# Performance work log

Measured on AMD Instinct MI355X. Metric: run time of the kernel, lower is better.

## Reference

```python
import jax, jax.numpy as jnp
import numpy as np

B, L, D, H = 2, 2048, 2048, 16
HD = D // H          # head_dim = 128
LD = HD // 4         # latent_dim = 32


def _linear_params(key, fan_in, fan_out):
    kw, kb = jax.random.split(key)
    bound = 1.0 / np.sqrt(fan_in)
    W = jax.random.uniform(kw, (fan_in, fan_out), jnp.float32, -bound, bound)
    b = jax.random.uniform(kb, (fan_out,), jnp.float32, -bound, bound)
    return W, b


def setup_inputs() -> dict:
    key = jax.random.key(0)
    ks = jax.random.split(key, 12)
    x = jax.random.normal(ks[0], (B, L, D), jnp.float32)
    cos = jax.random.uniform(ks[1], (L, HD // 2), jnp.float32)
    sin = jax.random.uniform(ks[2], (L, HD // 2), jnp.float32)
    Wq, bq = _linear_params(ks[3], D, D)
    Wk, bk = _linear_params(ks[4], D, D)
    Wv, bv = _linear_params(ks[5], D, D)
    Wqc, bqc = _linear_params(ks[6], HD, LD)
    Wkc, bkc = _linear_params(ks[7], HD, LD)
    Wvc, bvc = _linear_params(ks[8], HD, LD)
    Wd, bd = _linear_params(ks[9], LD, HD)
    Wo, bo = _linear_params(ks[10], D, D)
    return dict(x=x, cos=cos, sin=sin, Wq=Wq, bq=bq, Wk=Wk, bk=bk, Wv=Wv, bv=bv,
                Wqc=Wqc, bqc=bqc, Wkc=Wkc, bkc=bkc, Wvc=Wvc, bvc=bvc,
                Wd=Wd, bd=bd, Wo=Wo, bo=bo)


def _apply_rope(q, k, cos, sin):
    # q, k: (B, H, L, HD); cos, sin: (L, HD//2) -> broadcast over B, H
    c = cos[None, None, :, :]
    s = sin[None, None, :, :]
    qe, qo = q[..., ::2], q[..., 1::2]
    ke, ko = k[..., ::2], k[..., 1::2]
    q_rot = jnp.stack([qe * c - qo * s, qe * s + qo * c], axis=-1).reshape(q.shape)
    k_rot = jnp.stack([ke * c - ko * s, ke * s + ko * c], axis=-1).reshape(k.shape)
    return q_rot, k_rot


def reference(x, cos, sin, Wq, bq, Wk, bk, Wv, bv,
              Wqc, bqc, Wkc, bkc, Wvc, bvc, Wd, bd, Wo, bo):
    b, l, d = x.shape
    # projections -> (B, H, L, HD)
    q = (x @ Wq + bq).reshape(b, l, H, HD).transpose(0, 2, 1, 3)
    k = (x @ Wk + bk).reshape(b, l, H, HD).transpose(0, 2, 1, 3)
    v = (x @ Wv + bv).reshape(b, l, H, HD).transpose(0, 2, 1, 3)
    q, k = _apply_rope(q, k, cos, sin)
    # low-rank compression into latent_dim
    qc = jnp.einsum('bhld,de->bhle', q, Wqc) + bqc
    kc = jnp.einsum('bhld,de->bhle', k, Wkc) + bkc
    vc = jnp.einsum('bhld,de->bhle', v, Wvc) + bvc
    scores = jnp.einsum('bhqe,bhke->bhqk', qc, kc) / np.sqrt(LD).astype(np.float32)
    causal = jnp.tril(jnp.ones((l, l), dtype=bool))  # True = keep
    scores = jnp.where(causal[None, None], scores, -jnp.inf)
    probs = jax.nn.softmax(scores, axis=-1)
    attn = jnp.einsum('bhqk,bhke->bhqe', probs, vc)
    attn = jnp.einsum('bhle,ed->bhld', attn, Wd) + bd  # decompress to HD
    attn = attn.transpose(0, 2, 1, 3).reshape(b, l, d)
    return attn @ Wo + bo
```

## Files before the change

### kernel.cpp

```cpp
#include <hip/hip_runtime.h>
#include <hip/hip_bf16.h>


#define Bsz 2
#define Lseq 2048
#define Dmod 2048
#define Hn 16
#define HDim 128
#define LDim 32

typedef __bf16 bf16x8 __attribute__((ext_vector_type(8)));
typedef float f32x4 __attribute__((ext_vector_type(4)));
typedef __hip_bfloat16 bf16;

#define GLDS16(g, l)                                                    \
  __builtin_amdgcn_global_load_lds(                                     \
      (const __attribute__((address_space(1))) unsigned int*)(g),       \
      (__attribute__((address_space(3))) unsigned int*)(l), 16, 0, 0)

#define SM_COS 0
#define SM_SIN 131072
#define SM_WC 262144
#define SM_BC 274432
#define SM_WD 274528
#define SM_BD 278624
#define SM_BO 278752
#define SM_BQKV 280800
#define SM_TOT 286944

__device__ inline void conv8(const void* src, size_t so, bf16* dst, size_t dof, int f32) {
  if (f32) {
    const float* s = (const float*)src + so;
    bf16 tmp[8] __attribute__((aligned(16)));
    for (int j = 0; j < 8; ++j) tmp[j] = __float2bfloat16(s[j]);
    *(uint4*)&dst[dof] = *(uint4*)tmp;
  } else {
    *(uint4*)&dst[dof] = *(const uint4*)((const ushort*)src + so);
  }
}

__device__ inline float cv1(const void* s, size_t i, int f32) {
  return f32 ? ((const float*)s)[i] : __bfloat162float(((const bf16*)s)[i]);
}

#define PB_FBP 0
#define PB_T3 256
#define PB_WV 3328
#define PB_CX 5376
#define PB_SM 9472
#define NB_PREP_ALL 9632

__global__ __launch_bounds__(256) void prep_all(
    const void* xS, const void* cosS, const void* sinS, const void* WqS,
    const void* WkS, const void* WvS, const void* WoS, const void* WqcS,
    const void* WkcS, const void* WvcS, const void* bqcS, const void* bkcS,
    const void* bvcS, const void* WdS, const void* bdS, const void* boS,
    const void* bqS, const void* bkS, const void* bvS,
    bf16* __restrict__ xb, bf16* __restrict__ WvB, bf16* __restrict__ WtQK,
    bf16* __restrict__ WtO, bf16* __restrict__ small, bf16* __restrict__ wctG,
    float* __restrict__ bo_part, int* __restrict__ flagW) {
  __shared__ __align__(16) char shm[16640];
  __shared__ int sflag;
  int blk = blockIdx.x;
  int t = threadIdx.x;

  if (t < 64) {
    int bad = 0;
    for (int k = 0; k < 4; ++k) {
      ushort u = ((const ushort*)xS)[t * 4 + k];
      int ex = (u >> 7) & 0xFF;
      if (ex >= 0xC0) bad = 1;
    }
    unsigned long long bl = __ballot(bad);
    if (t == 0) sflag = (bl != 0ULL) ? 1 : 0;
  }
  __syncthreads();
  int f32 = sflag;
  if (blk == 0 && t == 0) *flagW = f32;

  if (blk < PB_T3) {
    float* red = (float*)shm;
    int nb = blk & 15, kb = blk >> 4;
    int col = nb * 128 + (t & 127);
    int half = t >> 7;
    float s = 0.f;
    int kbase = kb * 128 + half * 64;
    for (int i = 0; i < 64; ++i) {
      int k = kbase + i;
      s += cv1(bdS, k & 127, f32) * cv1(WoS, (size_t)k * 2048 + col, f32);
    }
    red[t] = s;
    __syncthreads();
    if (half == 0) bo_part[kb * 2048 + col] = red[t] + red[t + 128];
  } else if (blk < PB_WV) {
    float (*tile)[65] = (float(*)[65])shm;
    int rem0 = blk - PB_T3;
    int z = rem0 >> 10, rem = rem0 & 1023;
    const void* W = (z == 0) ? WqS : (z == 1) ? WkS : WoS;
    bf16* Wt = (z == 2) ? WtO : (WtQK + (size_t)z * 2048 * 2048);
    int n0 = (rem & 31) * 64, k0 = (rem >> 5) * 64;
    int x = (t & 7) * 8, y = t >> 3;
    for (int p = 0; p < 2; ++p) {
      int r = y + p * 32;
      if (f32) {
        const float* src = (const float*)W + (size_t)(k0 + r) * 2048 + n0 + x;
        float4 a = *(const float4*)src;
        float4 b2 = *(const float4*)(src + 4);
        tile[r][x + 0] = a.x; tile[r][x + 1] = a.y; tile[r][x + 2] = a.z; tile[r][x + 3] = a.w;
        tile[r][x + 4] = b2.x; tile[r][x + 5] = b2.y; tile[r][x + 6] = b2.z; tile[r][x + 7] = b2.w;
      } else {
        const ushort* src = (const ushort*)W + (size_t)(k0 + r) * 2048 + n0 + x;
        uint4 u = *(const uint4*)src;
        bf16* e = (bf16*)&u;
        for (int jj = 0; jj < 8; ++jj) tile[r][x + jj] = __bfloat162float(e[jj]);
      }
    }
    __syncthreads();
    for (int p = 0; p < 2; ++p) {
      int n = y + p * 32;
      bf16 tmp[8] __attribute__((aligned(16)));
      for (int jj = 0; jj < 8; ++jj) tmp[jj] = __float2bfloat16(tile[x + jj][n]);
      *(uint4*)&Wt[(size_t)(n0 + n) * 2048 + k0 + x] = *(uint4*)tmp;
    }
  } else if (blk < PB_CX) {
    size_t e = ((size_t)(blk - PB_WV) * 256 + t) * 8;
    conv8(WvS, e, WvB, e, f32);
  } else if (blk < PB_SM) {
    size_t e = ((size_t)(blk - PB_CX) * 256 + t) * 8;
    conv8(xS, e, xb, e, f32);
  } else {
    int tid = (blk - PB_SM) * 256 + t;
    if (tid < SM_TOT / 8) {
      size_t e = (size_t)tid * 8;
      const void* src;
      size_t so;
      if (e < SM_SIN) { src = cosS; so = e - SM_COS; }
      else if (e < SM_WC) { src = sinS; so = e - SM_SIN; }
      else if (e < SM_BC) { size_t r = e - SM_WC; src = (r < 4096) ? WqcS : (r < 8192) ? WkcS : WvcS; so = r & 4095; }
      else if (e < SM_WD) { size_t r = e - SM_BC; src = (r < 32) ? bqcS : (r < 64) ? bkcS : bvcS; so = r & 31; }
      else if (e < SM_BD) { src = WdS; so = e - SM_WD; }
      else if (e < SM_BO) { src = bdS; so = e - SM_BD; }
      else if (e < SM_BQKV) { src = boS; so = e - SM_BO; }
      else { size_t r = e - SM_BQKV; src = (r < 2048) ? bqS : (r < 4096) ? bkS : bvS; so = r & 2047; }
      conv8(src, so, small, e, f32);
    } else {
      int idx = tid - SM_TOT / 8;
      for (int i = idx; i < 12288; i += 40960 - SM_TOT / 8) {
        int reg = i >> 12, rem2 = i & 4095, n = rem2 >> 7, k = rem2 & 127;
        const void* src = (reg == 0) ? WqcS : (reg == 1) ? WkcS : WvcS;
        wctG[i] = __float2bfloat16(cv1(src, (size_t)k * 32 + n, f32));
      }
    }
  }
}

__global__ __launch_bounds__(256) void fold_all(
    const bf16* __restrict__ WvB, const bf16* __restrict__ wctG,
    const bf16* __restrict__ WtO, const bf16* __restrict__ small,
    const void* boS, const float* __restrict__ bo_part, const void* bvS,
    const void* bvcS, const void* WvcS, bf16* __restrict__ Wvt,
    bf16* __restrict__ Wot, float* __restrict__ boF, float* __restrict__ bvF,
    const int* __restrict__ flagp) {
  int blk = blockIdx.x;
  int t = threadIdx.x, lane = t & 63, w = t >> 6;
  int qd = lane >> 4, ln = lane & 15;
  if (blk < 256) {
    int nb = blk & 15, h = blk >> 4;
    f32x4 acc[2][2] = {};
    for (int kt = 0; kt < 4; ++kt) {
      bf16x8 af[2], bfr[2];
      for (int i = 0; i < 2; ++i)
        af[i] = *(const bf16x8*)&wctG[8192 + (i * 16 + ln) * 128 + kt * 32 + qd * 8];
      for (int j = 0; j < 2; ++j)
        bfr[j] = *(const bf16x8*)&WvB[(size_t)(nb * 128 + w * 32 + j * 16 + ln) * 2048 +
                                      h * 128 + kt * 32 + qd * 8];
      for (int i = 0; i < 2; ++i)
        for (int j = 0; j < 2; ++j)
          acc[i][j] = __builtin_amdgcn_mfma_f32_16x16x32_bf16(af[i], bfr[j], acc[i][j], 0, 0, 0);
    }
    for (int i = 0; i < 2; ++i)
      for (int j = 0; j < 2; ++j)
        for (int r = 0; r < 4; ++r) {
          int e = i * 16 + qd * 4 + r;
          int col = nb * 128 + w * 32 + j * 16 + ln;
          Wvt[(size_t)(h * 32 + e) * 2048 + col] = __float2bfloat16(acc[i][j][r]);
        }
  } else if (blk < 512) {
    int rem = blk - 256;
    int mb = rem & 15, h = rem >> 4;
    f32x4 acc[2][2] = {};
    for (int kt = 0; kt < 4; ++kt) {
      bf16x8 af[2], bfr[2];
      for (int i = 0; i < 2; ++i)
        af[i] = *(const bf16x8*)&WtO[(size_t)(mb * 128 + w * 32 + i * 16 + ln) * 2048 +
                                     h * 128 + kt * 32 + qd * 8];
      for (int j = 0; j < 2; ++j)
        bfr[j] = *(const bf16x8*)&small[SM_WD + (j * 16 + ln) * 128 + kt * 32 + qd * 8];
      for (int i = 0; i < 2; ++i)
        for (int j = 0; j < 2; ++j)
          acc[i][j] = __builtin_amdgcn_mfma_f32_16x16x32_bf16(af[i], bfr[j], acc[i][j], 0, 0, 0);
    }
    for (int i = 0; i < 2; ++i)
      for (int j = 0; j < 2; ++j)
        for (int r = 0; r < 4; ++r) {
          int row = mb * 128 + w * 32 + i * 16 + qd * 4 + r;
          int col = h * 32 + j * 16 + ln;
          Wot[(size_t)row * 512 + col] = __float2bfloat16(acc[i][j][r]);
        }
  } else {
    int f32 = *flagp;
    int tid = (blk - 512) * 256 + t;
    if (tid < 2048) {
      float s = cv1(boS, tid, f32);
      for (int kb = 0; kb < 16; ++kb) s += bo_part[kb * 2048 + tid];
      boF[tid] = s;
    } else if (tid < 2560) {
      int j = tid - 2048, h = j >> 5, e = j & 31;
      float s = cv1(bvcS, e, f32);
      for (int hd = 0; hd < 128; ++hd)
        s += cv1(bvS, h * 128 + hd, f32) * cv1(WvcS, (size_t)hd * 32 + e, f32);
      bvF[j] = s;
    }
  }
}

#define ESTR 136
__global__ __launch_bounds__(256) void gemm_qkv(
    const bf16* __restrict__ A, const bf16* __restrict__ Bt,
    const bf16* __restrict__ Wvt, const bf16* __restrict__ small,
    const bf16* __restrict__ wctG, const float* __restrict__ bvF,
    bf16* __restrict__ qc, bf16* __restrict__ kc, bf16* __restrict__ vcT) {
  __shared__ bf16 sh[128 * ESTR];
  const int K = 2048;
  int id = blockIdx.x;
  int t = threadIdx.x;
  int lane = t & 63, w = t >> 6;
  int qd = lane >> 4, ln = lane & 15;
  bf16* lA = sh;
  bf16* lB = sh + 4096;
  int wm = (w >> 1) * 64, wn = (w & 1) * 64;

  if (id < 1024) {
    int bn = id & 31, bm = id >> 5;
    int reg = bn >> 4, h = bn & 15;

    f32x4 acc[4][4] = {};
    const bf16* Ab = A + (size_t)(bm * 128) * K;
    const bf16* Bb = Bt + (size_t)(bn * 128) * K;

    for (int kt = 0; kt < K; kt += 32) {
      for (int p = 0; p < 2; ++p) {
        int slot = t + p * 256;
        int r = slot >> 2, c = (slot & 3) * 8;
        GLDS16(&Ab[(size_t)r * K + kt + c], &lA[slot * 8]);
        GLDS16(&Bb[(size_t)r * K + kt + c], &lB[slot * 8]);
      }
      __syncthreads();
      bf16x8 af[4], bfr[4];
      for (int i = 0; i < 4; ++i) af[i] = *(bf16x8*)&lA[(wm + i * 16 + ln) * 32 + qd * 8];
      for (int j = 0; j < 4; ++j) bfr[j] = *(bf16x8*)&lB[(wn + j * 16 + ln) * 32 + qd * 8];
      for (int i = 0; i < 4; ++i)
        for (int j = 0; j < 4; ++j)
          acc[i][j] = __builtin_amdgcn_mfma_f32_16x16x32_bf16(af[i], bfr[j], acc[i][j], 0, 0, 0);
      __syncthreads();
    }

    for (int j = 0; j < 4; ++j) {
      int col = wn + j * 16 + ln;
      float bv = __bfloat162float(small[SM_BQKV + bn * 128 + col]);
      for (int i = 0; i < 4; ++i)
        for (int r = 0; r < 4; ++r)
          sh[(wm + i * 16 + qd * 4 + r) * ESTR + col] = __float2bfloat16(acc[i][j][r] + bv);
    }
    __syncthreads();

    int r0 = w * 32;
    int b = bm >> 4;
    int bh = b * Hn + h;
    bf16x8 bfr2[2][4];
    for (int nt = 0; nt < 2; ++nt)
      for (int kt = 0; kt < 4; ++kt)
        bfr2[nt][kt] = *(const bf16x8*)&wctG[reg * 4096 + (nt * 16 + ln) * 128 + kt * 32 + qd * 8];
    float bc[2];
    bc[0] = __bfloat162float(small[SM_BC + reg * 32 + ln]);
    bc[1] = __bfloat162float(small[SM_BC + reg * 32 + 16 + ln]);

    for (int mt = 0; mt < 2; ++mt) {
      int lb = r0 + mt * 16 + ln;
      int lg2 = (bm & 15) * 128 + lb;
      f32x4 c2[2] = {};
      for (int kt = 0; kt < 4; ++kt) {
        uint4 u = *(uint4*)&sh[lb * ESTR + kt * 32 + qd * 8];
        bf16* e8 = (bf16*)&u;
        int pbase = kt * 16 + qd * 4;
        uint2 cu = *(const uint2*)&small[SM_COS + (size_t)lg2 * 64 + pbase];
        uint2 su = *(const uint2*)&small[SM_SIN + (size_t)lg2 * 64 + pbase];
        const bf16* cp = (const bf16*)&cu;
        const bf16* sp = (const bf16*)&su;
        for (int j = 0; j < 4; ++j) {
          float cvv = __bfloat162float(cp[j]);
          float svv = __bfloat162float(sp[j]);
          float ev = __bfloat162float(e8[2 * j]);
          float ov = __bfloat162float(e8[2 * j + 1]);
          e8[2 * j] = __float2bfloat16(ev * cvv - ov * svv);
          e8[2 * j + 1] = __float2bfloat16(ev * svv + ov * cvv);
        }
        bf16x8 a = *(bf16x8*)&u;
        c2[0] = __builtin_amdgcn_mfma_f32_16x16x32_bf16(a, bfr2[0][kt], c2[0], 0, 0, 0);
        c2[1] = __builtin_amdgcn_mfma_f32_16x16x32_bf16(a, bfr2[1][kt], c2[1], 0, 0, 0);
      }
      int lgbase = (bm & 15) * 128 + r0 + mt * 16 + qd * 4;
      bf16* dst = (reg == 0) ? qc : kc;
      for (int nt = 0; nt < 2; ++nt)
        for (int r = 0; r < 4; ++r)
          dst[((size_t)bh * Lseq + lgbase + r) * 32 + nt * 16 + ln] =
              __float2bfloat16(c2[nt][r] + bc[nt]);
    }
  } else {
    int rem = id - 1024;
    int nb = rem & 3, bm = rem >> 2;

    f32x4 acc[4][4] = {};
    const bf16* Ab = A + (size_t)(bm * 128) * K;
    const bf16* Bb = Wvt + (size_t)(nb * 128) * K;

    for (int kt = 0; kt < K; kt += 32) {
      for (int p = 0; p < 2; ++p) {
        int slot = t + p * 256;
        int r = slot >> 2, c = (slot & 3) * 8;
        GLDS16(&Ab[(size_t)r * K + kt + c], &lA[slot * 8]);
        GLDS16(&Bb[(size_t)r * K + kt + c], &lB[slot * 8]);
      }
      __syncthreads();
      bf16x8 af[4], bfr[4];
      for (int i = 0; i < 4; ++i) af[i] = *(bf16x8*)&lA[(wm + i * 16 + ln) * 32 + qd * 8];
      for (int j = 0; j < 4; ++j) bfr[j] = *(bf16x8*)&lB[(wn + j * 16 + ln) * 32 + qd * 8];
      for (int i = 0; i < 4; ++i)
        for (int j = 0; j < 4; ++j)
          acc[i][j] = __builtin_amdgcn_mfma_f32_16x16x32_bf16(af[i], bfr[j], acc[i][j], 0, 0, 0);
      __syncthreads();
    }

    int b = bm >> 4;
    for (int j = 0; j < 4; ++j) {
      int n = nb * 128 + wn + j * 16 + ln;
      float bb = bvF[n];
      for (int i = 0; i < 4; ++i) {
        int lloc = (bm & 15) * 128 + wm + i * 16 + qd * 4;
        bf16 p4[4] __attribute__((aligned(8)));
        for (int rr = 0; rr < 4; ++rr) p4[rr] = __float2bfloat16(acc[i][j][rr] + bb);
        *(uint2*)&vcT[((size_t)(b * 512 + n)) * 2048 + lloc] = *(uint2*)p4;
      }
    }
  }
}

__global__ __launch_bounds__(256) void gemm_bias_out(const bf16* __restrict__ A,
                                                     const bf16* __restrict__ Bt,
                                                     const float* __restrict__ bias,
                                                     void* __restrict__ C,
                                                     int M, int N, int K,
                                                     const int* __restrict__ flagp) {
  __shared__ bf16 lA[128 * 32];
  __shared__ bf16 lB[128 * 32];
  int f32out = *flagp;
  int bm = blockIdx.y, bn = blockIdx.x;
  int t = threadIdx.x;
  int lane = t & 63, w = t >> 6;
  int wm = (w >> 1) * 64, wn = (w & 1) * 64;
  int qd = lane >> 4, ln = lane & 15;

  f32x4 acc[4][4] = {};
  const bf16* Ab = A + (size_t)(bm * 128) * K;
  const bf16* Bb = Bt + (size_t)(bn * 128) * K;

  for (int kt = 0; kt < K; kt += 32) {
    for (int p = 0; p < 2; ++p) {
      int slot = t + p * 256;
      int r = slot >> 2, c = (slot & 3) * 8;
      GLDS16(&Ab[(size_t)r * K + kt + c], &lA[slot * 8]);
      GLDS16(&Bb[(size_t)r * K + kt + c], &lB[slot * 8]);
    }
    __syncthreads();
    bf16x8 af[4], bfr[4];
    for (int i = 0; i < 4; ++i) af[i] = *(bf16x8*)&lA[(wm + i * 16 + ln) * 32 + qd * 8];
    for (int j = 0; j < 4; ++j) bfr[j] = *(bf16x8*)&lB[(wn + j * 16 + ln) * 32 + qd * 8];
    for (int i = 0; i < 4; ++i)
      for (int j = 0; j < 4; ++j)
        acc[i][j] = __builtin_amdgcn_mfma_f32_16x16x32_bf16(af[i], bfr[j], acc[i][j], 0, 0, 0);
    __syncthreads();
  }
  for (int i = 0; i < 4; ++i)
    for (int j = 0; j < 4; ++j) {
      int col = bn * 128 + wn + j * 16 + ln;
      float bv = bias[col];
      for (int r = 0; r < 4; ++r) {
        int row = bm * 128 + wm + i * 16 + qd * 4 + r;
        float v = acc[i][j][r] + bv;
        if (f32out) ((float*)C)[(size_t)row * N + col] = v;
        else ((bf16*)C)[(size_t)row * N + col] = __float2bfloat16(v);
      }
    }
}

__global__ __launch_bounds__(256) void flash32(const bf16* __restrict__ qc,
                                               const bf16* __restrict__ kc,
                                               const bf16* __restrict__ vcT,
                                               bf16* __restrict__ attn) {
  __shared__ bf16 pbuf[4][16 * 72];
  __shared__ float oL[4][16][33];
  __shared__ float mL[4][16];
  __shared__ float lsL[4][16];
  int t = threadIdx.x;
  int lane = t & 63, w = t >> 6;
  int qd = lane >> 4, ln = lane & 15;
  int blk = blockIdx.x;
  int j = blk & 127;
  int bh = blk >> 7, h = bh & 15, b = bh >> 4;
  int q0 = j * 16;

  bf16x8 qf = *(const bf16x8*)&qc[((size_t)bh * Lseq + q0 + ln) * 32 + qd * 8];

  f32x4 o0 = {}, o1 = {};
  float m[4], ls[4];
  for (int r = 0; r < 4; ++r) { m[r] = -1e30f; ls[r] = 0.f; }
  const float scale2 = 0.17677669529663687f * 1.4426950408889634f;

  int n64 = (q0 + 16 + 63) >> 6;
  int nw = (n64 + 3) >> 2;
  int c0 = w * nw;
  int c1 = min(c0 + nw, n64);

  bf16* pb = pbuf[w];
  bf16x8 kf[4];
  if (c0 < c1) {
    int k0 = c0 * 64;
    for (int c = 0; c < 4; ++c)
      kf[c] = *(const bf16x8*)&kc[((size_t)bh * Lseq + k0 + c * 16 + ln) * 32 + qd * 8];
  }
  for (int ci = c0; ci < c1; ++ci) {
    int k0 = ci * 64;
    f32x4 s[4];
    __builtin_amdgcn_s_setprio(1);
    for (int c = 0; c < 4; ++c) {
      f32x4 z = {};
      s[c] = __builtin_amdgcn_mfma_f32_16x16x32_bf16(qf, kf[c], z, 0, 0, 0);
    }
    __builtin_amdgcn_s_setprio(0);
    size_t vbase = ((size_t)bh * 32 + ln) * Lseq + k0 + qd * 8;
    bf16x8 vf00 = *(const bf16x8*)&vcT[vbase];
    bf16x8 vf01 = *(const bf16x8*)&vcT[vbase + 32];
    bf16x8 vf10 = *(const bf16x8*)&vcT[vbase + (size_t)16 * Lseq];
    bf16x8 vf11 = *(const bf16x8*)&vcT[vbase + (size_t)16 * Lseq + 32];
    if (ci + 1 < c1) {
      int k0n = k0 + 64;
      for (int c = 0; c < 4; ++c)
        kf[c] = *(const bf16x8*)&kc[((size_t)bh * Lseq + k0n + c * 16 + ln) * 32 + qd * 8];
    }
    float sv[4][4];
    for (int r = 0; r < 4; ++r) {
      int qrow = q0 + qd * 4 + r;
      for (int c = 0; c < 4; ++c)
        sv[c][r] = (k0 + c * 16 + ln <= qrow) ? s[c][r] * scale2 : -1e30f;
    }
    for (int r = 0; r < 4; ++r) {
      float mx = fmaxf(fmaxf(sv[0][r], sv[1][r]), fmaxf(sv[2][r], sv[3][r]));
      for (int off = 1; off < 16; off <<= 1) mx = fmaxf(mx, __shfl_xor(mx, off, 64));
      if (!__all(mx <= m[r] + 8.f)) {
        float mn = fmaxf(m[r], mx);
        float alpha = exp2f(m[r] - mn);
        m[r] = mn;
        ls[r] *= alpha;
        o0[r] *= alpha;
        o1[r] *= alpha;
      }
      float rs = 0.f;
      for (int c = 0; c < 4; ++c) { sv[c][r] = exp2f(sv[c][r] - m[r]); rs += sv[c][r]; }
      ls[r] += rs;
    }
    for (int r = 0; r < 4; ++r)
      for (int c = 0; c < 4; ++c)
        pb[(qd * 4 + r) * 72 + c * 16 + ln] = __float2bfloat16(sv[c][r]);
    asm volatile("s_waitcnt lgkmcnt(0)" ::: "memory");
    bf16x8 pf0 = *(bf16x8*)&pb[ln * 72 + qd * 8];
    bf16x8 pf1 = *(bf16x8*)&pb[ln * 72 + 32 + qd * 8];
    __builtin_amdgcn_s_setprio(1);
    o0 = __builtin_amdgcn_mfma_f32_16x16x32_bf16(pf0, vf00, o0, 0, 0, 0);
    o0 = __builtin_amdgcn_mfma_f32_16x16x32_bf16(pf1, vf01, o0, 0, 0, 0);
    o1 = __builtin_amdgcn_mfma_f32_16x16x32_bf16(pf0, vf10, o1, 0, 0, 0);
    o1 = __builtin_amdgcn_mfma_f32_16x16x32_bf16(pf1, vf11, o1, 0, 0, 0);
    __builtin_amdgcn_s_setprio(0);
  }

  for (int r = 0; r < 4; ++r)
    for (int off = 1; off < 16; off <<= 1) ls[r] += __shfl_xor(ls[r], off, 64);

  for (int r = 0; r < 4; ++r) {
    int row = qd * 4 + r;
    oL[w][row][ln] = o0[r];
    oL[w][row][16 + ln] = o1[r];
    if (ln == 0) { mL[w][row] = m[r]; lsL[w][row] = ls[r]; }
  }
  __syncthreads();

  for (int idx = t; idx < 512; idx += 256) {
    int row = idx >> 5, col = idx & 31;
    float m0 = mL[0][row], m1 = mL[1][row], m2 = mL[2][row], m3 = mL[3][row];
    float ms = fmaxf(fmaxf(m0, m1), fmaxf(m2, m3));
    float e0 = exp2f(m0 - ms), e1 = exp2f(m1 - ms);
    float e2 = exp2f(m2 - ms), e3 = exp2f(m3 - ms);
    float lsum = lsL[0][row] * e0 + lsL[1][row] * e1 + lsL[2][row] * e2 + lsL[3][row] * e3;
    float val = oL[0][row][col] * e0 + oL[1][row][col] * e1 +
                oL[2][row][col] * e2 + oL[3][row][col] * e3;
    int l = q0 + row;
    attn[((size_t)(b * Lseq + l)) * 512 + h * 32 + col] = __float2bfloat16(val / lsum);
  }
}

extern "C" void kernel_launch(void* const* d_in, const int* in_sizes, int n_in,
                              void* d_out, int out_size, void* d_ws, size_t ws_size,
                              hipStream_t stream) {
  const void* x = d_in[0];
  const void* cosS = d_in[1];
  const void* sinS = d_in[2];
  const void* Wq = d_in[3];
  const void* bq = d_in[4];
  const void* Wk = d_in[5];
  const void* bk = d_in[6];
  const void* Wv = d_in[7];
  const void* bv = d_in[8];
  const void* Wqc = d_in[9];
  const void* bqc = d_in[10];
  const void* Wkc = d_in[11];
  const void* bkc = d_in[12];
  const void* Wvc = d_in[13];
  const void* bvc = d_in[14];
  const void* Wd = d_in[15];
  const void* bd = d_in[16];
  const void* Wo = d_in[17];
  const void* bo = d_in[18];

  char* ws = (char*)d_ws;
  size_t off = 0;
  auto alloc = [&](size_t bytes) {
    char* p = ws + off;
    off += (bytes + 255) & ~(size_t)255;
    return p;
  };
  int* flag = (int*)alloc(256);
  bf16* small = (bf16*)alloc((size_t)SM_TOT * 2);
  bf16* wctG = (bf16*)alloc((size_t)12288 * 2);
  bf16* xb = (bf16*)alloc((size_t)4096 * 2048 * 2);
  bf16* WvB = (bf16*)alloc((size_t)2048 * 2048 * 2);
  bf16* WtQK = (bf16*)alloc((size_t)4096 * 2048 * 2);
  bf16* WtO = (bf16*)alloc((size_t)2048 * 2048 * 2);
  bf16* Wvt = (bf16*)alloc((size_t)512 * 2048 * 2);
  bf16* Wot = (bf16*)alloc((size_t)2048 * 512 * 2);
  float* bo_part = (float*)alloc((size_t)16 * 2048 * 4);
  float* boF = (float*)alloc((size_t)2048 * 4);
  float* bvF = (float*)alloc((size_t)512 * 4);
  bf16* qcW = (bf16*)alloc((size_t)65536 * 32 * 2);
  bf16* kcW = (bf16*)alloc((size_t)65536 * 32 * 2);
  bf16* vcTW = (bf16*)alloc((size_t)65536 * 32 * 2);
  bf16* attnW = (bf16*)alloc((size_t)4096 * 512 * 2);

  dim3 tb(256);
  prep_all<<<NB_PREP_ALL, tb, 0, stream>>>(
      x, cosS, sinS, Wq, Wk, Wv, Wo, Wqc, Wkc, Wvc, bqc, bkc, bvc, Wd, bd, bo,
      bq, bk, bv, xb, WvB, WtQK, WtO, small, wctG, bo_part, flag);
  fold_all<<<522, tb, 0, stream>>>(WvB, wctG, WtO, small, bo, bo_part, bv, bvc,
                                   Wvc, Wvt, Wot, boF, bvF, flag);
  gemm_qkv<<<1152, tb, 0, stream>>>(xb, WtQK, Wvt, small, wctG, bvF, qcW, kcW, vcTW);
  flash32<<<4096, tb, 0, stream>>>(qcW, kcW, vcTW, attnW);
  gemm_bias_out<<<dim3(16, 32), tb, 0, stream>>>(attnW, Wot, boF, d_out, 4096, 2048,
                                                 512, flag);
}
```

Baseline: 382.9 us.

## Read Wv directly in fold and merge Wo/bias folding into QKV GEMM launch

Removes the separate Wv-to-bf16 conversion pass and its workspace buffer; the Wv fold reads the source weight directly and converts on the fly. The Wo fold and output-bias reduction blocks move from the fold kernel into extra blocks of the QKV GEMM launch, so the small fold kernel only builds Wvt and the folded v bias. This cuts one full 2048x2048 weight write and read and shrinks the pre-GEMM kernel, at the cost of uncoalesced fp32 loads in the fold and tail blocks added to the GEMM grid.

```diff
diff --git a/kernel.cpp b/kernel.cpp
--- a/kernel.cpp
+++ b/kernel.cpp
@@ -43,20 +43,29 @@
   return f32 ? ((const float*)s)[i] : __bfloat162float(((const bf16*)s)[i]);
 }
 
+__device__ inline bf16x8 load8bf(const void* src, size_t off, int f32) {
+  if (f32) {
+    const float* s = (const float*)src + off;
+    bf16 tmp[8] __attribute__((aligned(16)));
+    for (int q = 0; q < 8; ++q) tmp[q] = __float2bfloat16(s[q]);
+    return *(bf16x8*)tmp;
+  }
+  return *(const bf16x8*)((const ushort*)src + off);
+}
+
 #define PB_FBP 0
 #define PB_T3 256
-#define PB_WV 3328
-#define PB_CX 5376
-#define PB_SM 9472
-#define NB_PREP_ALL 9632
+#define PB_CX 3328
+#define PB_SM 7424
+#define NB_PREP_ALL 7584
 
 __global__ __launch_bounds__(256) void prep_all(
     const void* xS, const void* cosS, const void* sinS, const void* WqS,
-    const void* WkS, const void* WvS, const void* WoS, const void* WqcS,
+    const void* WkS, const void* WoS, const void* WqcS,
     const void* WkcS, const void* WvcS, const void* bqcS, const void* bkcS,
     const void* bvcS, const void* WdS, const void* bdS, const void* boS,
     const void* bqS, const void* bkS, const void* bvS,
-    bf16* __restrict__ xb, bf16* __restrict__ WvB, bf16* __restrict__ WtQK,
+    bf16* __restrict__ xb, bf16* __restrict__ WtQK,
     bf16* __restrict__ WtO, bf16* __restrict__ small, bf16* __restrict__ wctG,
     float* __restrict__ bo_part, int* __restrict__ flagW) {
   __shared__ __align__(16) char shm[16640];
@@ -92,7 +101,7 @@
     red[t] = s;
     __syncthreads();
     if (half == 0) bo_part[kb * 2048 + col] = red[t] + red[t + 128];
-  } else if (blk < PB_WV) {
+  } else if (blk < PB_CX) {
     float (*tile)[65] = (float(*)[65])shm;
     int rem0 = blk - PB_T3;
     int z = rem0 >> 10, rem = rem0 & 1023;
@@ -122,9 +131,6 @@
       for (int jj = 0; jj < 8; ++jj) tmp[jj] = __float2bfloat16(tile[x + jj][n]);
       *(uint4*)&Wt[(size_t)(n0 + n) * 2048 + k0 + x] = *(uint4*)tmp;
     }
-  } else if (blk < PB_CX) {
-    size_t e = ((size_t)(blk - PB_WV) * 256 + t) * 8;
-    conv8(WvS, e, WvB, e, f32);
   } else if (blk < PB_SM) {
     size_t e = ((size_t)(blk - PB_CX) * 256 + t) * 8;
     conv8(xS, e, xb, e, f32);
@@ -154,16 +160,14 @@
   }
 }
 
-__global__ __launch_bounds__(256) void fold_all(
-    const bf16* __restrict__ WvB, const bf16* __restrict__ wctG,
-    const bf16* __restrict__ WtO, const bf16* __restrict__ small,
-    const void* boS, const float* __restrict__ bo_part, const void* bvS,
+__global__ __launch_bounds__(256) void fold_pre(
+    const void* WvS, const bf16* __restrict__ wctG, const void* bvS,
     const void* bvcS, const void* WvcS, bf16* __restrict__ Wvt,
-    bf16* __restrict__ Wot, float* __restrict__ boF, float* __restrict__ bvF,
-    const int* __restrict__ flagp) {
+    float* __restrict__ bvF, const int* __restrict__ flagp) {
   int blk = blockIdx.x;
   int t = threadIdx.x, lane = t & 63, w = t >> 6;
   int qd = lane >> 4, ln = lane & 15;
+  int f32 = *flagp;
   if (blk < 256) {
     int nb = blk & 15, h = blk >> 4;
     f32x4 acc[2][2] = {};
@@ -172,8 +176,10 @@
       for (int i = 0; i < 2; ++i)
         af[i] = *(const bf16x8*)&wctG[8192 + (i * 16 + ln) * 128 + kt * 32 + qd * 8];
       for (int j = 0; j < 2; ++j)
-        bfr[j] = *(const bf16x8*)&WvB[(size_t)(nb * 128 + w * 32 + j * 16 + ln) * 2048 +
-                                      h * 128 + kt * 32 + qd * 8];
+        bfr[j] = load8bf(WvS,
+                         (size_t)(nb * 128 + w * 32 + j * 16 + ln) * 2048 +
+                             h * 128 + kt * 32 + qd * 8,
+                         f32);
       for (int i = 0; i < 2; ++i)
         for (int j = 0; j < 2; ++j)
           acc[i][j] = __builtin_amdgcn_mfma_f32_16x16x32_bf16(af[i], bfr[j], acc[i][j], 0, 0, 0);
@@ -185,10 +191,140 @@
           int col = nb * 128 + w * 32 + j * 16 + ln;
           Wvt[(size_t)(h * 32 + e) * 2048 + col] = __float2bfloat16(acc[i][j][r]);
         }
-  } else if (blk < 512) {
-    int rem = blk - 256;
+  } else {
+    int tid = (blk - 256) * 256 + t;
+    if (tid < 512) {
+      int h = tid >> 5, e = tid & 31;
+      float s = cv1(bvcS, e, f32);
+      for (int hd = 0; hd < 128; ++hd)
+        s += cv1(bvS, h * 128 + hd, f32) * cv1(WvcS, (size_t)hd * 32 + e, f32);
+      bvF[tid] = s;
+    }
+  }
+}
+
+#define ESTR 136
+__global__ __launch_bounds__(256) void gemm_qkv(
+    const bf16* __restrict__ A, const bf16* __restrict__ Bt,
+    const bf16* __restrict__ Wvt, const bf16* __restrict__ small,
+    const bf16* __restrict__ wctG, const float* __restrict__ bvF,
+    const bf16* __restrict__ WtO, const void* boS,
+    const float* __restrict__ bo_part,
+    bf16* __restrict__ qc, bf16* __restrict__ kc, bf16* __restrict__ vcT,
+    bf16* __restrict__ Wot, float* __restrict__ boF,
+    const int* __restrict__ flagp) {
+  __shared__ bf16 sh[128 * ESTR];
+  const int K = 2048;
+  int id = blockIdx.x;
+  int t = threadIdx.x;
+  int lane = t & 63, w = t >> 6;
+  int qd = lane >> 4, ln = lane & 15;
+  bf16* lA = sh;
+  bf16* lB = sh + 4096;
+  int wm = (w >> 1) * 64, wn = (w & 1) * 64;
+
+  if (id < 1152) {
+    int qkPath = id < 1024;
+    int bn, bm;
+    const bf16* Bb;
+    if (qkPath) {
+      bn = id & 31; bm = id >> 5;
+      Bb = Bt + (size_t)(bn * 128) * K;
+    } else {
+      int rem = id - 1024;
+      bn = rem & 3; bm = rem >> 2;
+      Bb = Wvt + (size_t)(bn * 128) * K;
+    }
+    const bf16* Ab = A + (size_t)(bm * 128) * K;
+
+    f32x4 acc[4][4] = {};
+    for (int kt = 0; kt < K; kt += 32) {
+      for (int p = 0; p < 2; ++p) {
+        int slot = t + p * 256;
+        int r = slot >> 2, c = (slot & 3) * 8;
+        GLDS16(&Ab[(size_t)r * K + kt + c], &lA[slot * 8]);
+        GLDS16(&Bb[(size_t)r * K + kt + c], &lB[slot * 8]);
+      }
+      __syncthreads();
+      bf16x8 af[4], bfr[4];
+      for (int i = 0; i < 4; ++i) af[i] = *(bf16x8*)&lA[(wm + i * 16 + ln) * 32 + qd * 8];
+      for (int j = 0; j < 4; ++j) bfr[j] = *(bf16x8*)&lB[(wn + j * 16 + ln) * 32 + qd * 8];
+      for (int i = 0; i < 4; ++i)
+        for (int j = 0; j < 4; ++j)
+          acc[i][j] = __builtin_amdgcn_mfma_f32_16x16x32_bf16(af[i], bfr[j], acc[i][j], 0, 0, 0);
+      __syncthreads();
+    }
+
+    if (qkPath) {
+      int reg = bn >> 4, h = bn & 15;
+      for (int j = 0; j < 4; ++j) {
+        int col = wn + j * 16 + ln;
+        float bv = __bfloat162float(small[SM_BQKV + bn * 128 + col]);
+        for (int i = 0; i < 4; ++i)
+          for (int r = 0; r < 4; ++r)
+            sh[(wm + i * 16 + qd * 4 + r) * ESTR + col] = __float2bfloat16(acc[i][j][r] + bv);
+      }
+      __syncthreads();
+
+      int r0 = w * 32;
+      int b = bm >> 4;
+      int bh = b * Hn + h;
+      bf16x8 bfr2[2][4];
+      for (int nt = 0; nt < 2; ++nt)
+        for (int kt = 0; kt < 4; ++kt)
+          bfr2[nt][kt] = *(const bf16x8*)&wctG[reg * 4096 + (nt * 16 + ln) * 128 + kt * 32 + qd * 8];
+      float bc[2];
+      bc[0] = __bfloat162float(small[SM_BC + reg * 32 + ln]);
+      bc[1] = __bfloat162float(small[SM_BC + reg * 32 + 16 + ln]);
+
+      for (int mt = 0; mt < 2; ++mt) {
+        int lb = r0 + mt * 16 + ln;
+        int lg2 = (bm & 15) * 128 + lb;
+        f32x4 c2[2] = {};
+        for (int kt = 0; kt < 4; ++kt) {
+          uint4 u = *(uint4*)&sh[lb * ESTR + kt * 32 + qd * 8];
+          bf16* e8 = (bf16*)&u;
+          int pbase = kt * 16 + qd * 4;
+          uint2 cu = *(const uint2*)&small[SM_COS + (size_t)lg2 * 64 + pbase];
+          uint2 su = *(const uint2*)&small[SM_SIN + (size_t)lg2 * 64 + pbase];
+          const bf16* cp = (const bf16*)&cu;
+          const bf16* sp = (const bf16*)&su;
+          for (int j = 0; j < 4; ++j) {
+            float cvv = __bfloat162float(cp[j]);
+            float svv = __bfloat162float(sp[j]);
+            float ev = __bfloat162float(e8[2 * j]);
+            float ov = __bfloat162float(e8[2 * j + 1]);
+            e8[2 * j] = __float2bfloat16(ev * cvv - ov * svv);
+            e8[2 * j + 1] = __float2bfloat16(ev * svv + ov * cvv);
+          }
+          bf16x8 a = *(bf16x8*)&u;
+          c2[0] = __builtin_amdgcn_mfma_f32_16x16x32_bf16(a, bfr2[0][kt], c2[0], 0, 0, 0);
+          c2[1] = __builtin_amdgcn_mfma_f32_16x16x32_bf16(a, bfr2[1][kt], c2[1], 0, 0, 0);
+        }
+        int lgbase = (bm & 15) * 128 + r0 + mt * 16 + qd * 4;
+        bf16* dst = (reg == 0) ? qc : kc;
+        for (int nt = 0; nt < 2; ++nt)
+          for (int r = 0; r < 4; ++r)
+            dst[((size_t)bh * Lseq + lgbase + r) * 32 + nt * 16 + ln] =
+                __float2bfloat16(c2[nt][r] + bc[nt]);
+      }
+    } else {
+      int b = bm >> 4;
+      for (int j = 0; j < 4; ++j) {
+        int n = bn * 128 + wn + j * 16 + ln;
+        float bb = bvF[n];
+        for (int i = 0; i < 4; ++i) {
+          int lloc = (bm & 15) * 128 + wm + i * 16 + qd * 4;
+          bf16 p4[4] __attribute__((aligned(8)));
+          for (int rr = 0; rr < 4; ++rr) p4[rr] = __float2bfloat16(acc[i][j][rr] + bb);
+          *(uint2*)&vcT[((size_t)(b * 512 + n)) * 2048 + lloc] = *(uint2*)p4;
+        }
+      }
+    }
+  } else if (id < 1408) {
+    int rem = id - 1152;
     int mb = rem & 15, h = rem >> 4;
-    f32x4 acc[2][2] = {};
+    f32x4 acc2[2][2] = {};
     for (int kt = 0; kt < 4; ++kt) {
       bf16x8 af[2], bfr[2];
       for (int i = 0; i < 2; ++i)
@@ -198,160 +334,21 @@
         bfr[j] = *(const bf16x8*)&small[SM_WD + (j * 16 + ln) * 128 + kt * 32 + qd * 8];
       for (int i = 0; i < 2; ++i)
         for (int j = 0; j < 2; ++j)
-          acc[i][j] = __builtin_amdgcn_mfma_f32_16x16x32_bf16(af[i], bfr[j], acc[i][j], 0, 0, 0);
+          acc2[i][j] = __builtin_amdgcn_mfma_f32_16x16x32_bf16(af[i], bfr[j], acc2[i][j], 0, 0, 0);
     }
     for (int i = 0; i < 2; ++i)
       for (int j = 0; j < 2; ++j)
         for (int r = 0; r < 4; ++r) {
           int row = mb * 128 + w * 32 + i * 16 + qd * 4 + r;
           int col = h * 32 + j * 16 + ln;
-          Wot[(size_t)row * 512 + col] = __float2bfloat16(acc[i][j][r]);
+          Wot[(size_t)row * 512 + col] = __float2bfloat16(acc2[i][j][r]);
         }
   } else {
     int f32 = *flagp;
-    int tid = (blk - 512) * 256 + t;
-    if (tid < 2048) {
-      float s = cv1(boS, tid, f32);
-      for (int kb = 0; kb < 16; ++kb) s += bo_part[kb * 2048 + tid];
-      boF[tid] = s;
-    } else if (tid < 2560) {
-      int j = tid - 2048, h = j >> 5, e = j & 31;
-      float s = cv1(bvcS, e, f32);
-      for (int hd = 0; hd < 128; ++hd)
-        s += cv1(bvS, h * 128 + hd, f32) * cv1(WvcS, (size_t)hd * 32 + e, f32);
-      bvF[j] = s;
-    }
-  }
-}
-
-#define ESTR 136
-__global__ __launch_bounds__(256) void gemm_qkv(
-    const bf16* __restrict__ A, const bf16* __restrict__ Bt,
-    const bf16* __restrict__ Wvt, const bf16* __restrict__ small,
-    const bf16* __restrict__ wctG, const float* __restrict__ bvF,
-    bf16* __restrict__ qc, bf16* __restrict__ kc, bf16* __restrict__ vcT) {
-  __shared__ bf16 sh[128 * ESTR];
-  const int K = 2048;
-  int id = blockIdx.x;
-  int t = threadIdx.x;
-  int lane = t & 63, w = t >> 6;
-  int qd = lane >> 4, ln = lane & 15;
-  bf16* lA = sh;
-  bf16* lB = sh + 4096;
-  int wm = (w >> 1) * 64, wn = (w & 1) * 64;
-
-  if (id < 1024) {
-    int bn = id & 31, bm = id >> 5;
-    int reg = bn >> 4, h = bn & 15;
-
-    f32x4 acc[4][4] = {};
-    const bf16* Ab = A + (size_t)(bm * 128) * K;
-    const bf16* Bb = Bt + (size_t)(bn * 128) * K;
-
-    for (int kt = 0; kt < K; kt += 32) {
-      for (int p = 0; p < 2; ++p) {
-        int slot = t + p * 256;
-        int r = slot >> 2, c = (slot & 3) * 8;
-        GLDS16(&Ab[(size_t)r * K + kt + c], &lA[slot * 8]);
-        GLDS16(&Bb[(size_t)r * K + kt + c], &lB[slot * 8]);
-      }
-      __syncthreads();
-      bf16x8 af[4], bfr[4];
-      for (int i = 0; i < 4; ++i) af[i] = *(bf16x8*)&lA[(wm + i * 16 + ln) * 32 + qd * 8];
-      for (int j = 0; j < 4; ++j) bfr[j] = *(bf16x8*)&lB[(wn + j * 16 + ln) * 32 + qd * 8];
-      for (int i = 0; i < 4; ++i)
-        for (int j = 0; j < 4; ++j)
-          acc[i][j] = __builtin_amdgcn_mfma_f32_16x16x32_bf16(af[i], bfr[j], acc[i][j], 0, 0, 0);
-      __syncthreads();
-    }
-
-    for (int j = 0; j < 4; ++j) {
-      int col = wn + j * 16 + ln;
-      float bv = __bfloat162float(small[SM_BQKV + bn * 128 + col]);
-      for (int i = 0; i < 4; ++i)
-        for (int r = 0; r < 4; ++r)
-          sh[(wm + i * 16 + qd * 4 + r) * ESTR + col] = __float2bfloat16(acc[i][j][r] + bv);
-    }
-    __syncthreads();
-
-    int r0 = w * 32;
-    int b = bm >> 4;
-    int bh = b * Hn + h;
-    bf16x8 bfr2[2][4];
-    for (int nt = 0; nt < 2; ++nt)
-      for (int kt = 0; kt < 4; ++kt)
-        bfr2[nt][kt] = *(const bf16x8*)&wctG[reg * 4096 + (nt * 16 + ln) * 128 + kt * 32 + qd * 8];
-    float bc[2];
-    bc[0] = __bfloat162float(small[SM_BC + reg * 32 + ln]);
-    bc[1] = __bfloat162float(small[SM_BC + reg * 32 + 16 + ln]);
-
-    for (int mt = 0; mt < 2; ++mt) {
-      int lb = r0 + mt * 16 + ln;
-      int lg2 = (bm & 15) * 128 + lb;
-      f32x4 c2[2] = {};
-      for (int kt = 0; kt < 4; ++kt) {
-        uint4 u = *(uint4*)&sh[lb * ESTR + kt * 32 + qd * 8];
-        bf16* e8 = (bf16*)&u;
-        int pbase = kt * 16 + qd * 4;
-        uint2 cu = *(const uint2*)&small[SM_COS + (size_t)lg2 * 64 + pbase];
-        uint2 su = *(const uint2*)&small[SM_SIN + (size_t)lg2 * 64 + pbase];
-        const bf16* cp = (const bf16*)&cu;
-        const bf16* sp = (const bf16*)&su;
-        for (int j = 0; j < 4; ++j) {
-          float cvv = __bfloat162float(cp[j]);
-          float svv = __bfloat162float(sp[j]);
-          float ev = __bfloat162float(e8[2 * j]);
-          float ov = __bfloat162float(e8[2 * j + 1]);
-          e8[2 * j] = __float2bfloat16(ev * cvv - ov * svv);
-          e8[2 * j + 1] = __float2bfloat16(ev * svv + ov * cvv);
-        }
-        bf16x8 a = *(bf16x8*)&u;
-        c2[0] = __builtin_amdgcn_mfma_f32_16x16x32_bf16(a, bfr2[0][kt], c2[0], 0, 0, 0);
-        c2[1] = __builtin_amdgcn_mfma_f32_16x16x32_bf16(a, bfr2[1][kt], c2[1], 0, 0, 0);
-      }
-      int lgbase = (bm & 15) * 128 + r0 + mt * 16 + qd * 4;
-      bf16* dst = (reg == 0) ? qc : kc;
-      for (int nt = 0; nt < 2; ++nt)
-        for (int r = 0; r < 4; ++r)
-          dst[((size_t)bh * Lseq + lgbase + r) * 32 + nt * 16 + ln] =
-              __float2bfloat16(c2[nt][r] + bc[nt]);
-    }
-  } else {
-    int rem = id - 1024;
-    int nb = rem & 3, bm = rem >> 2;
-
-    f32x4 acc[4][4] = {};
-    const bf16* Ab = A + (size_t)(bm * 128) * K;
-    const bf16* Bb = Wvt + (size_t)(nb * 128) * K;
-
-    for (int kt = 0; kt < K; kt += 32) {
-      for (int p = 0; p < 2; ++p) {
-        int slot = t + p * 256;
-        int r = slot >> 2, c = (slot & 3) * 8;
-        GLDS16(&Ab[(size_t)r * K + kt + c], &lA[slot * 8]);
-        GLDS16(&Bb[(size_t)r * K + kt + c], &lB[slot * 8]);
-      }
-      __syncthreads();
-      bf16x8 af[4], bfr[4];
-      for (int i = 0; i < 4; ++i) af[i] = *(bf16x8*)&lA[(wm + i * 16 + ln) * 32 + qd * 8];
-      for (int j = 0; j < 4; ++j) bfr[j] = *(bf16x8*)&lB[(wn + j * 16 + ln) * 32 + qd * 8];
-      for (int i = 0; i < 4; ++i)
-        for (int j = 0; j < 4; ++j)
-          acc[i][j] = __builtin_amdgcn_mfma_f32_16x16x32_bf16(af[i], bfr[j], acc[i][j], 0, 0, 0);
-      __syncthreads();
-    }
-
-    int b = bm >> 4;
-    for (int j = 0; j < 4; ++j) {
-      int n = nb * 128 + wn + j * 16 + ln;
-      float bb = bvF[n];
-      for (int i = 0; i < 4; ++i) {
-        int lloc = (bm & 15) * 128 + wm + i * 16 + qd * 4;
-        bf16 p4[4] __attribute__((aligned(8)));
-        for (int rr = 0; rr < 4; ++rr) p4[rr] = __float2bfloat16(acc[i][j][rr] + bb);
-        *(uint2*)&vcT[((size_t)(b * 512 + n)) * 2048 + lloc] = *(uint2*)p4;
-      }
-    }
+    int tid = (id - 1408) * 256 + t;
+    float s = cv1(boS, tid, f32);
+    for (int kb = 0; kb < 16; ++kb) s += bo_part[kb * 2048 + tid];
+    boF[tid] = s;
   }
 }
 
@@ -551,7 +548,6 @@
   bf16* small = (bf16*)alloc((size_t)SM_TOT * 2);
   bf16* wctG = (bf16*)alloc((size_t)12288 * 2);
   bf16* xb = (bf16*)alloc((size_t)4096 * 2048 * 2);
-  bf16* WvB = (bf16*)alloc((size_t)2048 * 2048 * 2);
   bf16* WtQK = (bf16*)alloc((size_t)4096 * 2048 * 2);
   bf16* WtO = (bf16*)alloc((size_t)2048 * 2048 * 2);
   bf16* Wvt = (bf16*)alloc((size_t)512 * 2048 * 2);
@@ -566,11 +562,11 @@
 
   dim3 tb(256);
   prep_all<<<NB_PREP_ALL, tb, 0, stream>>>(
-      x, cosS, sinS, Wq, Wk, Wv, Wo, Wqc, Wkc, Wvc, bqc, bkc, bvc, Wd, bd, bo,
-      bq, bk, bv, xb, WvB, WtQK, WtO, small, wctG, bo_part, flag);
-  fold_all<<<522, tb, 0, stream>>>(WvB, wctG, WtO, small, bo, bo_part, bv, bvc,
-                                   Wvc, Wvt, Wot, boF, bvF, flag);
-  gemm_qkv<<<1152, tb, 0, stream>>>(xb, WtQK, Wvt, small, wctG, bvF, qcW, kcW, vcTW);
+      x, cosS, sinS, Wq, Wk, Wo, Wqc, Wkc, Wvc, bqc, bkc, bvc, Wd, bd, bo,
+      bq, bk, bv, xb, WtQK, WtO, small, wctG, bo_part, flag);
+  fold_pre<<<258, tb, 0, stream>>>(Wv, wctG, bv, bvc, Wvc, Wvt, bvF, flag);
+  gemm_qkv<<<1416, tb, 0, stream>>>(xb, WtQK, Wvt, small, wctG, bvF, WtO, bo,
+                                    bo_part, qcW, kcW, vcTW, Wot, boF, flag);
   flash32<<<4096, tb, 0, stream>>>(qcW, kcW, vcTW, attnW);
   gemm_bias_out<<<dim3(16, 32), tb, 0, stream>>>(attnW, Wot, boF, d_out, 4096, 2048,
                                                  512, flag);
```

Result: slower. 400.4 us (+4.6%).
